# Performance work log

Hardware: AMD Instinct MI355X
Metric: run time of the kernel (lower is better)

Reference implementation:

```python
import jax, jax.numpy as jnp
import numpy as np

N = 33554432  # 2**25 elements
EPS = 1e-4    # keep probabilities strictly inside (0,1) to avoid log(0)

def setup_inputs() -> dict:
    key = jax.random.key(0)
    k1, k2 = jax.random.split(key)
    input_ = jax.random.uniform(k1, (N,), dtype=jnp.float32, minval=EPS, maxval=1.0 - EPS)
    target = jax.random.uniform(k2, (N,), dtype=jnp.float32, minval=EPS, maxval=1.0 - EPS)
    return {"input": input_, "target": target}

def reference(input, target):
    # Binary KL divergence per element, summed:
    # KL(p||q) = p*log(p/q) + (1-p)*log((1-p)/(1-q))
    p, q = input, target
    kl = p * (jnp.log(p) - jnp.log(q)) + (1.0 - p) * (jnp.log1p(-p) - jnp.log1p(-q))
    return kl.sum()
```

## Files before the change

kernel.cpp:

```cpp
#include <hip/hip_runtime.h>

#define BLOCK  256
#define GRID   2048
#define W4     1024
#define S4W    128
#define STAGES 8
#define RING   4

typedef float vfloat4 __attribute__((ext_vector_type(4)));

__device__ __forceinline__ void async_cp16(const vfloat4* g, vfloat4* lds_base) {
    __builtin_amdgcn_global_load_lds(
        (const __attribute__((address_space(1))) unsigned int*)g,
        (__attribute__((address_space(3))) unsigned int*)lds_base,
        16, 0, 0);
}

__device__ __forceinline__ void kl_acc(float p, float q, float& acc) {
    float omp = 1.0f - p;
    float omq = 1.0f - q;
    float d1  = __log2f(p)   - __log2f(q);
    float d2  = __log2f(omp) - __log2f(omq);
    acc = fmaf(p,   d1, acc);
    acc = fmaf(omp, d2, acc);
}

__device__ __forceinline__ void kl_acc4(vfloat4 pv, vfloat4 qv,
                                        float& a0, float& a1, float& a2, float& a3) {
    kl_acc(pv.x, qv.x, a0);
    kl_acc(pv.y, qv.y, a1);
    kl_acc(pv.z, qv.z, a2);
    kl_acc(pv.w, qv.w, a3);
}

__device__ __forceinline__ void block_reduce_and_atomic(float acc, float* out) {
    const float LN2 = 0.69314718055994530942f;
    #pragma unroll
    for (int off = 32; off > 0; off >>= 1)
        acc += __shfl_down(acc, off, 64);

    __shared__ float wave_sums[BLOCK / 64];
    const int lane = threadIdx.x & 63;
    const int wave = threadIdx.x >> 6;
    if (lane == 0) wave_sums[wave] = acc;
    __syncthreads();

    if (threadIdx.x == 0) {
        float s = 0.0f;
        #pragma unroll
        for (int w = 0; w < BLOCK / 64; ++w) s += wave_sums[w];
        atomicAdd(out, s * LN2);
    }
}

__global__ __launch_bounds__(BLOCK, 4) void kl_div_ring(
        const vfloat4* __restrict__ p4,
        const vfloat4* __restrict__ q4,
        float* __restrict__ out) {
    __shared__ vfloat4 sp[4][RING][S4W];

    const int t    = threadIdx.x;
    const int w    = t >> 6;
    const int lane = t & 63;
    const size_t wbase = ((size_t)blockIdx.x * 4 + w) * W4;

    vfloat4 qr[RING][2];
    float a0 = 0.0f, a1 = 0.0f, a2 = 0.0f, a3 = 0.0f;

    #define ISSUE(S) do {                                                  \
        const size_t g0 = wbase + (size_t)(S) * S4W + lane;                \
        vfloat4* dst = &sp[w][(S) & (RING - 1)][0];                        \
        async_cp16(p4 + g0,      dst);                                     \
        async_cp16(p4 + g0 + 64, dst + 64);                                \
        qr[(S) & (RING - 1)][0] = __builtin_nontemporal_load(q4 + g0);     \
        qr[(S) & (RING - 1)][1] = __builtin_nontemporal_load(q4 + g0 + 64);\
    } while (0)

    #define STEP(S, VM) do {                                               \
        if ((S) + 3 < STAGES) ISSUE((S) + 3);                              \
        __builtin_amdgcn_sched_barrier(0);                                 \
        __builtin_amdgcn_s_waitcnt((VM) | 0x70 | 0xF00);                   \
        asm volatile("" ::: "memory");                                     \
        __builtin_amdgcn_sched_barrier(0);                                 \
        vfloat4 pv0 = sp[w][(S) & (RING - 1)][lane];                       \
        vfloat4 pv1 = sp[w][(S) & (RING - 1)][lane + 64];                  \
        kl_acc4(pv0, qr[(S) & (RING - 1)][0], a0, a1, a2, a3);             \
        kl_acc4(pv1, qr[(S) & (RING - 1)][1], a0, a1, a2, a3);             \
    } while (0)

    ISSUE(0); ISSUE(1); ISSUE(2);
    STEP(0, 12); STEP(1, 12); STEP(2, 12); STEP(3, 12);
    STEP(4, 12); STEP(5, 8);  STEP(6, 4);  STEP(7, 0);

    #undef STEP
    #undef ISSUE

    float acc = (a0 + a1) + (a2 + a3);
    block_reduce_and_atomic(acc, out);
}

__global__ __launch_bounds__(BLOCK) void kl_div_generic(
        const float* __restrict__ p,
        const float* __restrict__ q,
        float* __restrict__ out,
        int n) {
    const int nvec = n >> 2;
    const vfloat4* __restrict__ p4 = reinterpret_cast<const vfloat4*>(p);
    const vfloat4* __restrict__ q4 = reinterpret_cast<const vfloat4*>(q);

    float acc = 0.0f;
    const int stride = gridDim.x * blockDim.x;
    for (int i = blockIdx.x * blockDim.x + threadIdx.x; i < nvec; i += stride) {
        vfloat4 pv = p4[i];
        vfloat4 qv = q4[i];
        kl_acc(pv.x, qv.x, acc);
        kl_acc(pv.y, qv.y, acc);
        kl_acc(pv.z, qv.z, acc);
        kl_acc(pv.w, qv.w, acc);
    }
    for (int i = (nvec << 2) + blockIdx.x * blockDim.x + threadIdx.x; i < n; i += stride) {
        kl_acc(p[i], q[i], acc);
    }
    block_reduce_and_atomic(acc, out);
}

extern "C" void kernel_launch(void* const* d_in, const int* in_sizes, int n_in,
                              void* d_out, int out_size, void* d_ws, size_t ws_size,
                              hipStream_t stream) {
    const float* p = (const float*)d_in[0];
    const float* q = (const float*)d_in[1];
    float* out = (float*)d_out;
    const int n = in_sizes[0];

    hipMemsetAsync(out, 0, sizeof(float), stream);

    if (n == GRID * 4 * W4 * 4) {
        kl_div_ring<<<GRID, BLOCK, 0, stream>>>(
            reinterpret_cast<const vfloat4*>(p),
            reinterpret_cast<const vfloat4*>(q), out);
    } else {
        kl_div_generic<<<GRID, BLOCK, 0, stream>>>(p, q, out, n);
    }
}
```

Measured before the change: 262.1 us.

## Replace LDS async ring pipeline with simple grid-strided vector loads

Removes the hand-scheduled ring that staged p through LDS via global_load_lds with manual waitcnt control. Each thread now loops 16 times over grid-strided float4 loads of p and q, unrolled by 4, with occupancy hinted at 8 blocks per CU. This drops the LDS traffic and explicit waits and relies on the compiler and hardware to keep enough loads in flight. The trade-off is less explicit control over latency hiding and ordinary cached loads instead of nontemporal ones for q.

```diff
diff --git a/kernel.cpp b/kernel.cpp
--- a/kernel.cpp
+++ b/kernel.cpp
@@ -1,20 +1,10 @@
 #include <hip/hip_runtime.h>
 
-#define BLOCK  256
-#define GRID   2048
-#define W4     1024
-#define S4W    128
-#define STAGES 8
-#define RING   4
+#define BLOCK 256
+#define GRID  2048
+#define ITERS 16
 
 typedef float vfloat4 __attribute__((ext_vector_type(4)));
-
-__device__ __forceinline__ void async_cp16(const vfloat4* g, vfloat4* lds_base) {
-    __builtin_amdgcn_global_load_lds(
-        (const __attribute__((address_space(1))) unsigned int*)g,
-        (__attribute__((address_space(3))) unsigned int*)lds_base,
-        16, 0, 0);
-}
 
 __device__ __forceinline__ void kl_acc(float p, float q, float& acc) {
     float omp = 1.0f - p;
@@ -53,47 +43,22 @@
     }
 }
 
-__global__ __launch_bounds__(BLOCK, 4) void kl_div_ring(
+__global__ __launch_bounds__(BLOCK, 8) void kl_div_stream(
         const vfloat4* __restrict__ p4,
         const vfloat4* __restrict__ q4,
         float* __restrict__ out) {
-    __shared__ vfloat4 sp[4][RING][S4W];
+    const int    tid    = blockIdx.x * BLOCK + threadIdx.x;
+    const size_t stride = (size_t)GRID * BLOCK;
 
-    const int t    = threadIdx.x;
-    const int w    = t >> 6;
-    const int lane = t & 63;
-    const size_t wbase = ((size_t)blockIdx.x * 4 + w) * W4;
-
-    vfloat4 qr[RING][2];
     float a0 = 0.0f, a1 = 0.0f, a2 = 0.0f, a3 = 0.0f;
 
-    #define ISSUE(S) do {                                                  \
-        const size_t g0 = wbase + (size_t)(S) * S4W + lane;                \
-        vfloat4* dst = &sp[w][(S) & (RING - 1)][0];                        \
-        async_cp16(p4 + g0,      dst);                                     \
-        async_cp16(p4 + g0 + 64, dst + 64);                                \
-        qr[(S) & (RING - 1)][0] = __builtin_nontemporal_load(q4 + g0);     \
-        qr[(S) & (RING - 1)][1] = __builtin_nontemporal_load(q4 + g0 + 64);\
-    } while (0)
-
-    #define STEP(S, VM) do {                                               \
-        if ((S) + 3 < STAGES) ISSUE((S) + 3);                              \
-        __builtin_amdgcn_sched_barrier(0);                                 \
-        __builtin_amdgcn_s_waitcnt((VM) | 0x70 | 0xF00);                   \
-        asm volatile("" ::: "memory");                                     \
-        __builtin_amdgcn_sched_barrier(0);                                 \
-        vfloat4 pv0 = sp[w][(S) & (RING - 1)][lane];                       \
-        vfloat4 pv1 = sp[w][(S) & (RING - 1)][lane + 64];                  \
-        kl_acc4(pv0, qr[(S) & (RING - 1)][0], a0, a1, a2, a3);             \
-        kl_acc4(pv1, qr[(S) & (RING - 1)][1], a0, a1, a2, a3);             \
-    } while (0)
-
-    ISSUE(0); ISSUE(1); ISSUE(2);
-    STEP(0, 12); STEP(1, 12); STEP(2, 12); STEP(3, 12);
-    STEP(4, 12); STEP(5, 8);  STEP(6, 4);  STEP(7, 0);
-
-    #undef STEP
-    #undef ISSUE
+    #pragma unroll 4
+    for (int k = 0; k < ITERS; ++k) {
+        const size_t i = (size_t)k * stride + tid;
+        vfloat4 pv = p4[i];
+        vfloat4 qv = q4[i];
+        kl_acc4(pv, qv, a0, a1, a2, a3);
+    }
 
     float acc = (a0 + a1) + (a2 + a3);
     block_reduce_and_atomic(acc, out);
@@ -134,8 +99,8 @@
 
     hipMemsetAsync(out, 0, sizeof(float), stream);
 
-    if (n == GRID * 4 * W4 * 4) {
-        kl_div_ring<<<GRID, BLOCK, 0, stream>>>(
+    if (n == GRID * BLOCK * ITERS * 4) {
+        kl_div_stream<<<GRID, BLOCK, 0, stream>>>(
             reinterpret_cast<const vfloat4*>(p),
             reinterpret_cast<const vfloat4*>(q), out);
     } else {
```

After: 278.6 us. 6.3% more time.
